# Optimization experiments

Hardware: AMD Instinct MI355X
Metric: run time of the kernel (lower is better)

The kernel has to match this reference:

```python
import jax, jax.numpy as jnp
import numpy as np

B, T, I, H, O = 32, 2048, 128, 256, 64


def setup_inputs() -> dict:
    key = jax.random.key(0)
    ks = jax.random.split(key, 7)
    s = 0.05
    return {
        "x": jax.random.normal(ks[0], (B, T, I), dtype=jnp.float32),
        # PyTorch LSTM params (single layer): gate order i, f, g, o
        "W_ih": jax.random.normal(ks[1], (4 * H, I), dtype=jnp.float32) * s,
        "W_hh": jax.random.normal(ks[2], (4 * H, H), dtype=jnp.float32) * s,
        "b_ih": jax.random.normal(ks[3], (4 * H,), dtype=jnp.float32) * s,
        "b_hh": jax.random.normal(ks[4], (4 * H,), dtype=jnp.float32) * s,
        "W_fc": jax.random.normal(ks[5], (O, H), dtype=jnp.float32) * s,
        "b_fc": jax.random.normal(ks[6], (O,), dtype=jnp.float32) * s,
    }


def _lstm(x, W_ih, W_hh, b_ih, b_hh):
    # x: (B, T, I) -> hidden states (B, T, H). PyTorch gate order i,f,g,o.
    Bn, Tn, _ = x.shape
    Hn = W_hh.shape[1]
    # Precompute input projection once (memory-bound friendly):
    x_proj = jnp.einsum("bti,gi->btg", x, W_ih) + b_ih + b_hh  # (B, T, 4H)
    x_proj = jnp.swapaxes(x_proj, 0, 1)  # (T, B, 4H)

    def step(carry, xt):
        h, c = carry
        gates = xt + h @ W_hh.T  # (B, 4H)
        i, f, g, o = jnp.split(gates, 4, axis=-1)
        i = jax.nn.sigmoid(i)
        f = jax.nn.sigmoid(f)
        g = jnp.tanh(g)
        o = jax.nn.sigmoid(o)
        c = f * c + i * g
        h = o * jnp.tanh(c)
        return (h, c), h

    h0 = jnp.zeros((Bn, Hn), dtype=x.dtype)
    c0 = jnp.zeros((Bn, Hn), dtype=x.dtype)
    _, hs = jax.lax.scan(step, (h0, c0), x_proj)  # (T, B, H)
    return jnp.swapaxes(hs, 0, 1)  # (B, T, H)


def reference(x, W_ih, W_hh, b_ih, b_hh, W_fc, b_fc):
    h = _lstm(x, W_ih, W_hh, b_ih, b_hh)          # (B, T, H)
    logits = jnp.einsum("bth,oh->bto", h, W_fc) + b_fc  # fused fc over all (b,t)
    # original applies softmax over the feature vector at each (i, j)
    return jax.nn.softmax(logits, axis=-1)        # (B, T, O)
```

## Files before the change

### kernel.cpp

```cpp
#include <hip/hip_runtime.h>
#include <hip/hip_bf16.h>
#include <hip/hip_fp16.h>

typedef _Float16 v2h __attribute__((ext_vector_type(2)));

__device__ __forceinline__ float fdot2u(unsigned int a, unsigned int b, float c){
  return __builtin_amdgcn_fdot2(__builtin_bit_cast(v2h, a), __builtin_bit_cast(v2h, b), c, false);
}
__device__ __forceinline__ unsigned int packh2(float a, float b){
  union{ _Float16 h[2]; unsigned int u; } z;
  z.h[0] = (_Float16)a; z.h[1] = (_Float16)b; return z.u;
}
__device__ __forceinline__ float h2f(unsigned short s){
  return (float)__builtin_bit_cast(_Float16, s);
}
__device__ __forceinline__ float sigf(float x){
  return __builtin_amdgcn_rcpf(1.0f + __builtin_amdgcn_exp2f(-1.44269504f*x));
}
__device__ __forceinline__ float tanhf_(float x){
  return 2.0f*__builtin_amdgcn_rcpf(1.0f + __builtin_amdgcn_exp2f(-2.88539008f*x)) - 1.0f;
}
__device__ __forceinline__ float dpp_xor1(float x){
  return __builtin_bit_cast(float,
    __builtin_amdgcn_mov_dpp(__builtin_bit_cast(int, x), 0xB1, 0xF, 0xF, true));
}
__device__ __forceinline__ float dpp_xor2(float x){
  return __builtin_bit_cast(float,
    __builtin_amdgcn_mov_dpp(__builtin_bit_cast(int, x), 0x4E, 0xF, 0xF, true));
}

__global__ void prep_kernel(const float* __restrict__ Whh, const float* __restrict__ Wfc,
                            const float* __restrict__ bih, const float* __restrict__ bhh,
                            unsigned int* __restrict__ whhT2, unsigned int* __restrict__ wfc16,
                            float* __restrict__ bsum){
  int i = blockIdx.x*256 + threadIdx.x;
  if (i < 131072){
    int r = i >> 7, d = i & 127;
    int g = r >> 8, u = r & 255;
    int p = d >> 5, j = (d >> 2) & 7, l = d & 3;
    whhT2[(size_t)((g*8+j)*1024 + u*4 + p)*4 + l] = packh2(Whh[r*256 + 2*d], Whh[r*256 + 2*d + 1]);
  } else if (i < 139264){
    int j = i - 131072; int o = j >> 7, d = j & 127;
    wfc16[j] = packh2(Wfc[o*256 + 2*d], Wfc[o*256 + 2*d + 1]);
  } else if (i < 140288){
    int g = i - 139264;
    bsum[g] = bih[g] + bhh[g];
  }
}

#define XS 68
__global__ __launch_bounds__(256) void xproj_kernel(const float* __restrict__ x,
                          const float* __restrict__ Wih,
                          const float* __restrict__ bsum, unsigned int* __restrict__ xproj){
  __shared__ unsigned int lx[128*XS];
  __shared__ unsigned int lw[64*XS];
  __shared__ float lb[64];
  int t  = threadIdx.x;
  int bt0 = blockIdx.x*128, g0 = blockIdx.y*64;
  int rr = t >> 4, cc = t & 15;
  #pragma unroll
  for (int it=0; it<8; ++it){
    int row = rr + it*16;
    const float4* s = (const float4*)(x + (size_t)(bt0+row)*128 + cc*8);
    float4 a = s[0], b = s[1];
    uint4 w; w.x=packh2(a.x,a.y); w.y=packh2(a.z,a.w); w.z=packh2(b.x,b.y); w.w=packh2(b.z,b.w);
    *(uint4*)&lx[row*XS + cc*4] = w;
  }
  #pragma unroll
  for (int it=0; it<4; ++it){
    int row = rr + it*16;
    const float4* s = (const float4*)(Wih + (size_t)(g0+row)*128 + cc*8);
    float4 a = s[0], b = s[1];
    uint4 w; w.x=packh2(a.x,a.y); w.y=packh2(a.z,a.w); w.z=packh2(b.x,b.y); w.w=packh2(b.z,b.w);
    *(uint4*)&lw[row*XS + cc*4] = w;
  }
  if (t < 64) lb[t] = bsum[g0 + t];
  __syncthreads();

  float acc[8][4];
  #pragma unroll
  for (int j=0;j<8;++j)
    #pragma unroll
    for (int i=0;i<4;++i) acc[j][i]=0.f;

  #pragma unroll
  for (int d4=0; d4<16; ++d4){
    uint4 wv[4], xv[8];
    #pragma unroll
    for (int i=0;i<4;++i) wv[i] = *(const uint4*)&lw[(cc*4+i)*XS + d4*4];
    #pragma unroll
    for (int j=0;j<8;++j) xv[j] = *(const uint4*)&lx[(rr*8+j)*XS + d4*4];
    #pragma unroll
    for (int j=0;j<8;++j){
      #pragma unroll
      for (int i=0;i<4;++i){
        float a = acc[j][i];
        a = fdot2u(xv[j].x, wv[i].x, a);
        a = fdot2u(xv[j].y, wv[i].y, a);
        a = fdot2u(xv[j].z, wv[i].z, a);
        a = fdot2u(xv[j].w, wv[i].w, a);
        acc[j][i] = a;
      }
    }
  }
  #pragma unroll
  for (int j=0;j<8;++j){
    int bt = bt0 + rr*8 + j;
    uint2 o2;
    o2.x = packh2(acc[j][0]+lb[cc*4+0], acc[j][1]+lb[cc*4+1]);
    o2.y = packh2(acc[j][2]+lb[cc*4+2], acc[j][3]+lb[cc*4+3]);
    *(uint2*)&xproj[(size_t)bt*512 + (g0>>1) + cc*2] = o2;
  }
}

#define WL4 8
#define HOFF (WL4*4096)
#define HBUF 528

extern "C" __global__ void __launch_bounds__(1024,4) lstm_kernel(
    const unsigned int* __restrict__ whhT2, const unsigned int* __restrict__ xproj,
    unsigned short* __restrict__ h_all)
{
  extern __shared__ unsigned int lds[];
  uint4* lw4 = (uint4*)lds;
  unsigned short* lds16 = (unsigned short*)lds;
  const int t = threadIdx.x;
  const int u = t >> 2, p = t & 3;
  const int b = blockIdx.x;
  const int p164 = p*164;

  const uint4* wsrc = (const uint4*)whhT2;
  uint4 w4[3][8];
  #pragma unroll
  for (int g=0; g<3; ++g)
    #pragma unroll
    for (int j=0; j<8; ++j) w4[g][j] = wsrc[(g*8+j)*1024 + t];
  #pragma unroll
  for (int q=0; q<WL4; ++q) lw4[q*1024 + t] = wsrc[(24+q)*1024 + t];
  if (t < HBUF) lds[HOFF + t] = 0u;

  const float m0 = (p==0)?1.f:0.f, m1 = (p==1)?1.f:0.f,
              m2 = (p==2)?1.f:0.f, m3 = (p==3)?1.f:0.f;
  const unsigned short* xpb = (const unsigned short*)xproj + (size_t)b*2048*1024;
  const int xoff = p*256 + u;
  unsigned short xn = xpb[xoff];
  float c = 0.f;
  unsigned short* hout = h_all + (size_t)b*2048*256 + u;
  __syncthreads();

  for (int tt=0; tt<2048; ++tt){
    const int cur = tt & 1;
    float A0 = 0.f, A1 = 0.f, A2 = 0.f, A3 = 0.f;
    float xv = h2f(xn);
    int tn = (tt+1 < 2048) ? tt+1 : 2047;
    xn = xpb[(size_t)tn*1024 + xoff];

    const unsigned int* hb = lds + HOFF + cur*HBUF + p164;
    #pragma unroll
    for (int j=0; j<8; ++j){
      uint4 h4 = *(const uint4*)(hb + j*4);
      uint4 wo = lw4[j*1024 + t];
      A0 = fdot2u(w4[0][j].x, h4.x, A0); A0 = fdot2u(w4[0][j].y, h4.y, A0);
      A0 = fdot2u(w4[0][j].z, h4.z, A0); A0 = fdot2u(w4[0][j].w, h4.w, A0);
      A1 = fdot2u(w4[1][j].x, h4.x, A1); A1 = fdot2u(w4[1][j].y, h4.y, A1);
      A1 = fdot2u(w4[1][j].z, h4.z, A1); A1 = fdot2u(w4[1][j].w, h4.w, A1);
      A2 = fdot2u(w4[2][j].x, h4.x, A2); A2 = fdot2u(w4[2][j].y, h4.y, A2);
      A2 = fdot2u(w4[2][j].z, h4.z, A2); A2 = fdot2u(w4[2][j].w, h4.w, A2);
      A3 = fdot2u(wo.x, h4.x, A3); A3 = fdot2u(wo.y, h4.y, A3);
      A3 = fdot2u(wo.z, h4.z, A3); A3 = fdot2u(wo.w, h4.w, A3);
    }
    A0 = fmaf(m0, xv, A0); A1 = fmaf(m1, xv, A1);
    A2 = fmaf(m2, xv, A2); A3 = fmaf(m3, xv, A3);
    A0 += dpp_xor1(A0); A1 += dpp_xor1(A1);
    A2 += dpp_xor1(A2); A3 += dpp_xor1(A3);
    A0 += dpp_xor2(A0); A1 += dpp_xor2(A1);
    A2 += dpp_xor2(A2); A3 += dpp_xor2(A3);

    float gi = sigf(A0);
    float gf = sigf(A1);
    float gg = tanhf_(A2);
    float go = sigf(A3);
    c = gf*c + gi*gg;
    float h = go * tanhf_(c);
    unsigned short hh = __builtin_bit_cast(unsigned short, (_Float16)h);
    lds16[(HOFF + (cur^1)*HBUF + p*132)*2 + u] = hh;
    if (p == 0) hout[(size_t)tt*256] = hh;
    __syncthreads();
  }
}

__global__ __launch_bounds__(1024) void fc_softmax_kernel(const unsigned short* __restrict__ h_all,
      const unsigned int* __restrict__ wfc16, const float* __restrict__ bfc,
      float* __restrict__ out){
  __shared__ unsigned int lwf[64*132];
  __shared__ unsigned int lh[16*132];
  int t = threadIdx.x;
  int bt0 = blockIdx.x*16;
  {
    const uint4* s = (const uint4*)(wfc16 + (size_t)t*8);
    uint4 a = s[0], b = s[1];
    unsigned int* dst = &lwf[(t>>4)*132 + (t&15)*8];
    *(uint4*)dst = a; *(uint4*)(dst+4) = b;
  }
  {
    int row = t>>6, col = (t&63)*2;
    const unsigned int* hsrc = (const unsigned int*)h_all;
    uint2 v = *(const uint2*)(hsrc + (size_t)(bt0+row)*128 + col);
    *(uint2*)&lh[row*132 + col] = v;
  }
  __syncthreads();
  int w = t>>6, o = t&63;
  int bt = bt0 + w;
  float acc = bfc[o];
  #pragma unroll
  for (int d4=0; d4<32; ++d4){
    uint4 hq = *(const uint4*)&lh[w*132 + d4*4];
    uint4 wq = *(const uint4*)&lwf[o*132 + d4*4];
    acc = fdot2u(wq.x, hq.x, acc);
    acc = fdot2u(wq.y, hq.y, acc);
    acc = fdot2u(wq.z, hq.z, acc);
    acc = fdot2u(wq.w, hq.w, acc);
  }
  float m = acc;
  #pragma unroll
  for (int off=32; off>=1; off>>=1) m = fmaxf(m, __shfl_xor(m, off));
  float e = __builtin_amdgcn_exp2f(1.44269504f*(acc - m));
  float s = e;
  #pragma unroll
  for (int off=32; off>=1; off>>=1) s += __shfl_xor(s, off);
  out[(size_t)bt*64 + o] = e * __builtin_amdgcn_rcpf(s);
}

extern "C" void kernel_launch(void* const* d_in, const int* in_sizes, int n_in,
                              void* d_out, int out_size, void* d_ws, size_t ws_size,
                              hipStream_t stream){
  const float* x   = (const float*)d_in[0];
  const float* Wih = (const float*)d_in[1];
  const float* Whh = (const float*)d_in[2];
  const float* bih = (const float*)d_in[3];
  const float* bhh = (const float*)d_in[4];
  const float* Wfc = (const float*)d_in[5];
  const float* bfc = (const float*)d_in[6];
  float* out = (float*)d_out;

  char* ws = (char*)d_ws;
  unsigned int*   xproj = (unsigned int*)ws;
  unsigned short* h_all = (unsigned short*)(ws + 134217728);
  unsigned int*   whhT2 = (unsigned int*)(ws + 134217728 + 33554432);
  unsigned int*   wfc16 = whhT2 + 131072;
  float*          bsum  = (float*)(wfc16 + 8192);

  prep_kernel<<<548, 256, 0, stream>>>(Whh, Wfc, bih, bhh, whhT2, wfc16, bsum);
  dim3 gb(512, 16);
  xproj_kernel<<<gb, 256, 0, stream>>>(x, Wih, bsum, xproj);
  int dyn = (HOFF + 2*HBUF) * 4;
  hipFuncSetAttribute((const void*)lstm_kernel, hipFuncAttributeMaxDynamicSharedMemorySize, dyn);
  lstm_kernel<<<32, 1024, dyn, stream>>>(whhT2, xproj, h_all);
  fc_softmax_kernel<<<4096, 1024, 0, stream>>>(h_all, wfc16, bfc, out);
}
```

Measured before the change: 3.355 ms.

## Stream most output-gate weights from global/L2 each step instead of LDS

Shrinks the LDS-resident share of the output-gate recurrent weights from 8 to 2 uint4 slices per thread. The remaining 6 slices are reloaded from global memory (expected to hit L2/cache) every timestep, issued early so the loads overlap the dot products. An asm barrier stops the compiler from hoisting these loads out of the loop. The aim is to cut LDS footprint and LDS bandwidth pressure in the serial recurrence, at the cost of per-step global load latency on the critical path.

```diff
diff --git a/kernel.cpp b/kernel.cpp
--- a/kernel.cpp
+++ b/kernel.cpp
@@ -113,9 +113,20 @@
   }
 }
 
-#define WL4 8
+#define WL4 2
 #define HOFF (WL4*4096)
 #define HBUF 528
+
+#define DOTJ(J, WO) { \
+    uint4 h4 = *(const uint4*)(hb + (J)*4); \
+    A0 = fdot2u(w4[0][J].x, h4.x, A0); A0 = fdot2u(w4[0][J].y, h4.y, A0); \
+    A0 = fdot2u(w4[0][J].z, h4.z, A0); A0 = fdot2u(w4[0][J].w, h4.w, A0); \
+    A1 = fdot2u(w4[1][J].x, h4.x, A1); A1 = fdot2u(w4[1][J].y, h4.y, A1); \
+    A1 = fdot2u(w4[1][J].z, h4.z, A1); A1 = fdot2u(w4[1][J].w, h4.w, A1); \
+    A2 = fdot2u(w4[2][J].x, h4.x, A2); A2 = fdot2u(w4[2][J].y, h4.y, A2); \
+    A2 = fdot2u(w4[2][J].z, h4.z, A2); A2 = fdot2u(w4[2][J].w, h4.w, A2); \
+    A3 = fdot2u((WO).x, h4.x, A3); A3 = fdot2u((WO).y, h4.y, A3); \
+    A3 = fdot2u((WO).z, h4.z, A3); A3 = fdot2u((WO).w, h4.w, A3); }
 
 extern "C" __global__ void __launch_bounds__(1024,4) lstm_kernel(
     const unsigned int* __restrict__ whhT2, const unsigned int* __restrict__ xproj,
@@ -139,6 +150,8 @@
   for (int q=0; q<WL4; ++q) lw4[q*1024 + t] = wsrc[(24+q)*1024 + t];
   if (t < HBUF) lds[HOFF + t] = 0u;
 
+  const unsigned long long gbase = (unsigned long long)(wsrc + 26*1024 + t);
+
   const float m0 = (p==0)?1.f:0.f, m1 = (p==1)?1.f:0.f,
               m2 = (p==2)?1.f:0.f, m3 = (p==3)?1.f:0.f;
   const unsigned short* xpb = (const unsigned short*)xproj + (size_t)b*2048*1024;
@@ -150,25 +163,35 @@
 
   for (int tt=0; tt<2048; ++tt){
     const int cur = tt & 1;
+    unsigned long long ga = gbase;
+    asm volatile("" : "+v"(ga));
+    const uint4* gp = (const uint4*)ga;
+    uint4 wg0 = gp[0*1024];
+    uint4 wg1 = gp[1*1024];
+    uint4 wg2 = gp[2*1024];
+    uint4 wg3 = gp[3*1024];
+
     float A0 = 0.f, A1 = 0.f, A2 = 0.f, A3 = 0.f;
     float xv = h2f(xn);
     int tn = (tt+1 < 2048) ? tt+1 : 2047;
     xn = xpb[(size_t)tn*1024 + xoff];
 
     const unsigned int* hb = lds + HOFF + cur*HBUF + p164;
-    #pragma unroll
-    for (int j=0; j<8; ++j){
-      uint4 h4 = *(const uint4*)(hb + j*4);
-      uint4 wo = lw4[j*1024 + t];
-      A0 = fdot2u(w4[0][j].x, h4.x, A0); A0 = fdot2u(w4[0][j].y, h4.y, A0);
-      A0 = fdot2u(w4[0][j].z, h4.z, A0); A0 = fdot2u(w4[0][j].w, h4.w, A0);
-      A1 = fdot2u(w4[1][j].x, h4.x, A1); A1 = fdot2u(w4[1][j].y, h4.y, A1);
-      A1 = fdot2u(w4[1][j].z, h4.z, A1); A1 = fdot2u(w4[1][j].w, h4.w, A1);
-      A2 = fdot2u(w4[2][j].x, h4.x, A2); A2 = fdot2u(w4[2][j].y, h4.y, A2);
-      A2 = fdot2u(w4[2][j].z, h4.z, A2); A2 = fdot2u(w4[2][j].w, h4.w, A2);
-      A3 = fdot2u(wo.x, h4.x, A3); A3 = fdot2u(wo.y, h4.y, A3);
-      A3 = fdot2u(wo.z, h4.z, A3); A3 = fdot2u(wo.w, h4.w, A3);
+    {
+      uint4 wo0 = lw4[0*1024 + t];
+      DOTJ(0, wo0);
+      uint4 wo1 = lw4[1*1024 + t];
+      DOTJ(1, wo1);
     }
+    DOTJ(2, wg0);
+    uint4 wg4 = gp[4*1024];
+    DOTJ(3, wg1);
+    uint4 wg5 = gp[5*1024];
+    DOTJ(4, wg2);
+    DOTJ(5, wg3);
+    DOTJ(6, wg4);
+    DOTJ(7, wg5);
+
     A0 = fmaf(m0, xv, A0); A1 = fmaf(m1, xv, A1);
     A2 = fmaf(m2, xv, A2); A3 = fmaf(m3, xv, A3);
     A0 += dpp_xor1(A0); A1 += dpp_xor1(A1);
```

Result: slower. 4.635 ms (+38.1%).

## Repartition LSTM recurrence to 512 threads with two lanes per hidden unit

Applied to the files above, without the earlier changes.

The recurrent kernel now uses 512 threads per sequence, with two lanes per hidden unit instead of four. Each lane computes all four gates over half the hidden vector, which halves the cross-lane reduction to one DPP step. The W_hh layout changes to match: 13 of 16 chunks per gate stay in registers and 3 go to LDS, loaded up front before the register-resident loop. Fewer waves should make each per-step barrier cheaper, but each thread does twice the dot-product work, and register pressure may be high.

```diff
diff --git a/kernel.cpp b/kernel.cpp
--- a/kernel.cpp
+++ b/kernel.cpp
@@ -24,21 +24,17 @@
   return __builtin_bit_cast(float,
     __builtin_amdgcn_mov_dpp(__builtin_bit_cast(int, x), 0xB1, 0xF, 0xF, true));
 }
-__device__ __forceinline__ float dpp_xor2(float x){
-  return __builtin_bit_cast(float,
-    __builtin_amdgcn_mov_dpp(__builtin_bit_cast(int, x), 0x4E, 0xF, 0xF, true));
-}
 
 __global__ void prep_kernel(const float* __restrict__ Whh, const float* __restrict__ Wfc,
                             const float* __restrict__ bih, const float* __restrict__ bhh,
-                            unsigned int* __restrict__ whhT2, unsigned int* __restrict__ wfc16,
+                            unsigned int* __restrict__ whhT3, unsigned int* __restrict__ wfc16,
                             float* __restrict__ bsum){
   int i = blockIdx.x*256 + threadIdx.x;
   if (i < 131072){
     int r = i >> 7, d = i & 127;
     int g = r >> 8, u = r & 255;
-    int p = d >> 5, j = (d >> 2) & 7, l = d & 3;
-    whhT2[(size_t)((g*8+j)*1024 + u*4 + p)*4 + l] = packh2(Whh[r*256 + 2*d], Whh[r*256 + 2*d + 1]);
+    int p = (d >> 6) & 1, j = (d >> 2) & 15, l = d & 3;
+    whhT3[(size_t)((g*16+j)*512 + u*2 + p)*4 + l] = packh2(Whh[r*256 + 2*d], Whh[r*256 + 2*d + 1]);
   } else if (i < 139264){
     int j = i - 131072; int o = j >> 7, d = j & 127;
     wfc16[j] = packh2(Wfc[o*256 + 2*d], Wfc[o*256 + 2*d + 1]);
@@ -113,68 +109,98 @@
   }
 }
 
-#define WL4 8
-#define HOFF (WL4*4096)
-#define HBUF 528
-
-extern "C" __global__ void __launch_bounds__(1024,4) lstm_kernel(
-    const unsigned int* __restrict__ whhT2, const unsigned int* __restrict__ xproj,
+#define WRJ 13
+#define WLJ 3
+#define HOFF (4*WLJ*512*4)
+
+extern "C" __global__ void __launch_bounds__(512,2) lstm_kernel(
+    const unsigned int* __restrict__ whhT3, const unsigned int* __restrict__ xproj,
     unsigned short* __restrict__ h_all)
 {
   extern __shared__ unsigned int lds[];
   uint4* lw4 = (uint4*)lds;
   unsigned short* lds16 = (unsigned short*)lds;
   const int t = threadIdx.x;
-  const int u = t >> 2, p = t & 3;
+  const int u = t >> 1, p = t & 1;
   const int b = blockIdx.x;
-  const int p164 = p*164;
-
-  const uint4* wsrc = (const uint4*)whhT2;
-  uint4 w4[3][8];
-  #pragma unroll
-  for (int g=0; g<3; ++g)
-    #pragma unroll
-    for (int j=0; j<8; ++j) w4[g][j] = wsrc[(g*8+j)*1024 + t];
-  #pragma unroll
-  for (int q=0; q<WL4; ++q) lw4[q*1024 + t] = wsrc[(24+q)*1024 + t];
-  if (t < HBUF) lds[HOFF + t] = 0u;
-
-  const float m0 = (p==0)?1.f:0.f, m1 = (p==1)?1.f:0.f,
-              m2 = (p==2)?1.f:0.f, m3 = (p==3)?1.f:0.f;
+
+  const uint4* wsrc = (const uint4*)whhT3;
+  uint4 w0[WRJ], w1[WRJ], w2[WRJ], w3[WRJ];
+  #pragma unroll
+  for (int j=0; j<WRJ; ++j){
+    w0[j] = wsrc[(0*16+j)*512 + t];
+    w1[j] = wsrc[(1*16+j)*512 + t];
+    w2[j] = wsrc[(2*16+j)*512 + t];
+    w3[j] = wsrc[(3*16+j)*512 + t];
+  }
+  #pragma unroll
+  for (int g=0; g<4; ++g)
+    #pragma unroll
+    for (int jj=0; jj<WLJ; ++jj)
+      lw4[(g*WLJ+jj)*512 + t] = wsrc[(g*16+WRJ+jj)*512 + t];
+  if (t < 256) lds[HOFF + t] = 0u;
+
+  const float mp = (p==0) ? 1.f : 0.f;
   const unsigned short* xpb = (const unsigned short*)xproj + (size_t)b*2048*1024;
-  const int xoff = p*256 + u;
-  unsigned short xn = xpb[xoff];
+  unsigned short xn0 = xpb[u], xn1 = xpb[256+u], xn2 = xpb[512+u], xn3 = xpb[768+u];
   float c = 0.f;
   unsigned short* hout = h_all + (size_t)b*2048*256 + u;
   __syncthreads();
 
   for (int tt=0; tt<2048; ++tt){
     const int cur = tt & 1;
+    float xv0 = h2f(xn0), xv1 = h2f(xn1), xv2 = h2f(xn2), xv3 = h2f(xn3);
+    int tn = (tt+1 < 2048) ? tt+1 : 2047;
+    {
+      const unsigned short* xr = xpb + (size_t)tn*1024;
+      xn0 = xr[u]; xn1 = xr[256+u]; xn2 = xr[512+u]; xn3 = xr[768+u];
+    }
     float A0 = 0.f, A1 = 0.f, A2 = 0.f, A3 = 0.f;
-    float xv = h2f(xn);
-    int tn = (tt+1 < 2048) ? tt+1 : 2047;
-    xn = xpb[(size_t)tn*1024 + xoff];
-
-    const unsigned int* hb = lds + HOFF + cur*HBUF + p164;
-    #pragma unroll
-    for (int j=0; j<8; ++j){
+    const unsigned int* hb = lds + HOFF + cur*128 + p*64;
+
+    int zoff = 0;
+    asm volatile("" : "+v"(zoff));
+    const uint4* lwl = lw4 + zoff;
+
+    uint4 h4s[WLJ], wg0[WLJ], wg1[WLJ], wg2[WLJ], wg3[WLJ];
+    #pragma unroll
+    for (int jj=0; jj<WLJ; ++jj){
+      h4s[jj] = *(const uint4*)(hb + (WRJ+jj)*4);
+      wg0[jj] = lwl[(0*WLJ+jj)*512 + t];
+      wg1[jj] = lwl[(1*WLJ+jj)*512 + t];
+      wg2[jj] = lwl[(2*WLJ+jj)*512 + t];
+      wg3[jj] = lwl[(3*WLJ+jj)*512 + t];
+    }
+
+    #pragma unroll
+    for (int j=0; j<WRJ; ++j){
       uint4 h4 = *(const uint4*)(hb + j*4);
-      uint4 wo = lw4[j*1024 + t];
-      A0 = fdot2u(w4[0][j].x, h4.x, A0); A0 = fdot2u(w4[0][j].y, h4.y, A0);
-      A0 = fdot2u(w4[0][j].z, h4.z, A0); A0 = fdot2u(w4[0][j].w, h4.w, A0);
-      A1 = fdot2u(w4[1][j].x, h4.x, A1); A1 = fdot2u(w4[1][j].y, h4.y, A1);
-      A1 = fdot2u(w4[1][j].z, h4.z, A1); A1 = fdot2u(w4[1][j].w, h4.w, A1);
-      A2 = fdot2u(w4[2][j].x, h4.x, A2); A2 = fdot2u(w4[2][j].y, h4.y, A2);
-      A2 = fdot2u(w4[2][j].z, h4.z, A2); A2 = fdot2u(w4[2][j].w, h4.w, A2);
-      A3 = fdot2u(wo.x, h4.x, A3); A3 = fdot2u(wo.y, h4.y, A3);
-      A3 = fdot2u(wo.z, h4.z, A3); A3 = fdot2u(wo.w, h4.w, A3);
-    }
-    A0 = fmaf(m0, xv, A0); A1 = fmaf(m1, xv, A1);
-    A2 = fmaf(m2, xv, A2); A3 = fmaf(m3, xv, A3);
+      A0 = fdot2u(w0[j].x, h4.x, A0); A0 = fdot2u(w0[j].y, h4.y, A0);
+      A0 = fdot2u(w0[j].z, h4.z, A0); A0 = fdot2u(w0[j].w, h4.w, A0);
+      A1 = fdot2u(w1[j].x, h4.x, A1); A1 = fdot2u(w1[j].y, h4.y, A1);
+      A1 = fdot2u(w1[j].z, h4.z, A1); A1 = fdot2u(w1[j].w, h4.w, A1);
+      A2 = fdot2u(w2[j].x, h4.x, A2); A2 = fdot2u(w2[j].y, h4.y, A2);
+      A2 = fdot2u(w2[j].z, h4.z, A2); A2 = fdot2u(w2[j].w, h4.w, A2);
+      A3 = fdot2u(w3[j].x, h4.x, A3); A3 = fdot2u(w3[j].y, h4.y, A3);
+      A3 = fdot2u(w3[j].z, h4.z, A3); A3 = fdot2u(w3[j].w, h4.w, A3);
+    }
+    #pragma unroll
+    for (int jj=0; jj<WLJ; ++jj){
+      uint4 h4 = h4s[jj];
+      A0 = fdot2u(wg0[jj].x, h4.x, A0); A0 = fdot2u(wg0[jj].y, h4.y, A0);
+      A0 = fdot2u(wg0[jj].z, h4.z, A0); A0 = fdot2u(wg0[jj].w, h4.w, A0);
+      A1 = fdot2u(wg1[jj].x, h4.x, A1); A1 = fdot2u(wg1[jj].y, h4.y, A1);
+      A1 = fdot2u(wg1[jj].z, h4.z, A1); A1 = fdot2u(wg1[jj].w, h4.w, A1);
+      A2 = fdot2u(wg2[jj].x, h4.x, A2); A2 = fdot2u(wg2[jj].y, h4.y, A2);
+      A2 = fdot2u(wg2[jj].z, h4.z, A2); A2 = fdot2u(wg2[jj].w, h4.w, A2);
+      A3 = fdot2u(wg3[jj].x, h4.x, A3); A3 = fdot2u(wg3[jj].y, h4.y, A3);
+      A3 = fdot2u(wg3[jj].z, h4.z, A3); A3 = fdot2u(wg3[jj].w, h4.w, A3);
+    }
+
+    A0 = fmaf(mp, xv0, A0); A1 = fmaf(mp, xv1, A1);
+    A2 = fmaf(mp, xv2, A2); A3 = fmaf(mp, xv3, A3);
     A0 += dpp_xor1(A0); A1 += dpp_xor1(A1);
     A2 += dpp_xor1(A2); A3 += dpp_xor1(A3);
-    A0 += dpp_xor2(A0); A1 += dpp_xor2(A1);
-    A2 += dpp_xor2(A2); A3 += dpp_xor2(A3);
 
     float gi = sigf(A0);
     float gf = sigf(A1);
@@ -183,8 +209,10 @@
     c = gf*c + gi*gg;
     float h = go * tanhf_(c);
     unsigned short hh = __builtin_bit_cast(unsigned short, (_Float16)h);
-    lds16[(HOFF + (cur^1)*HBUF + p*132)*2 + u] = hh;
-    if (p == 0) hout[(size_t)tt*256] = hh;
+    if (p == 0){
+      lds16[(HOFF + (cur^1)*128)*2 + u] = hh;
+      hout[(size_t)tt*256] = hh;
+    }
     __syncthreads();
   }
 }
@@ -246,15 +274,15 @@
   char* ws = (char*)d_ws;
   unsigned int*   xproj = (unsigned int*)ws;
   unsigned short* h_all = (unsigned short*)(ws + 134217728);
-  unsigned int*   whhT2 = (unsigned int*)(ws + 134217728 + 33554432);
-  unsigned int*   wfc16 = whhT2 + 131072;
+  unsigned int*   whhT3 = (unsigned int*)(ws + 134217728 + 33554432);
+  unsigned int*   wfc16 = whhT3 + 131072;
   float*          bsum  = (float*)(wfc16 + 8192);
 
-  prep_kernel<<<548, 256, 0, stream>>>(Whh, Wfc, bih, bhh, whhT2, wfc16, bsum);
+  prep_kernel<<<548, 256, 0, stream>>>(Whh, Wfc, bih, bhh, whhT3, wfc16, bsum);
   dim3 gb(512, 16);
   xproj_kernel<<<gb, 256, 0, stream>>>(x, Wih, bsum, xproj);
-  int dyn = (HOFF + 2*HBUF) * 4;
+  int dyn = (HOFF + 256) * 4;
   hipFuncSetAttribute((const void*)lstm_kernel, hipFuncAttributeMaxDynamicSharedMemorySize, dyn);
-  lstm_kernel<<<32, 1024, dyn, stream>>>(whhT2, xproj, h_all);
+  lstm_kernel<<<32, 512, dyn, stream>>>(whhT3, xproj, h_all);
   fc_softmax_kernel<<<4096, 1024, 0, stream>>>(h_all, wfc16, bfc, out);
 }
```

Result: faster. 3.043 ms (-9.3%).
